# Optimization experiments

Measured on AMD Instinct MI355X. Metric: run time of the kernel, lower is better.

The kernel has to match this reference:

```python
import jax, jax.numpy as jnp
from jax import lax
import numpy as np

EPS = 1e-10
LAMBDA = 0.7  # adaptive_attention_selector: H=64>16 -> 0.0, then C=320>64 -> max(0.0, 0.7)


def delu(x, p=10.0):
    # p*relu(x) + (exp(p*min(x,0)) - 1) + 1  ==  p*relu(x) + exp(p*(x - relu(x)))
    x1 = jax.nn.relu(x)
    return p * x1 + jnp.exp(p * (x - x1))


def conv1x1(x, w, b):
    # x: (B,C,H,W), w: (O,C), b: (O,)
    return jnp.einsum('oc,bchw->bohw', w, x) + b[None, :, None, None]


def conv3x3(x, w, b):
    y = lax.conv_general_dilated(x, w, (1, 1), ((1, 1), (1, 1)),
                                 dimension_numbers=('NCHW', 'OIHW', 'NCHW'))
    return y + b[None, :, None, None]


def _forward(swin_feat, resnet_feat, w_swin, b_swin, w_res, b_res,
             aq_w, aq_b, ak_w, ak_b, av_w, av_b, ad1_w, ad1_b, ad3_w, ad3_b, a_gamma,
             lq_w, lq_b, lk_w, lk_b, lv_w, lv_b, ld1_w, ld1_b, ld3_w, ld3_b, l_gamma,
             wc_w, wc_b):
    sa = conv1x1(swin_feat, w_swin, b_swin)
    ra = conv1x1(resnet_feat, w_res, b_res)
    x = jnp.concatenate([sa, ra], axis=1)           # (B, C=320, H, W)
    B, C, H, W = x.shape
    N = H * W

    # ---- SelfAttentionV1 (softmax bmm output is dead code in the source; only the kv path survives) ----
    q = jnp.swapaxes(conv1x1(x, aq_w, aq_b).reshape(B, -1, N), 1, 2)   # (B, N, C8)
    k = conv1x1(x, ak_w, ak_b).reshape(B, -1, N)                        # (B, C8, N)
    v = conv1x1(x, av_w, av_b).reshape(B, C, N)                         # (B, C, N)
    kv = jnp.einsum('bmn,bcn->bmc', k, v)                               # (B, C8, C)
    norm = 1.0 / jnp.einsum('bnc,bc->bn', q, jnp.sum(k, axis=-1) + EPS) # (B, N)
    wv = jnp.einsum('bnm,bmc,bn->bcn', q, kv, norm).reshape(B, C, H, W)
    d1 = conv1x1(x, ad1_w, ad1_b)
    d3 = conv3x3(x, ad3_w, ad3_b)
    # weight_value = wv + d1 + d3; out = weight_value + d1 + d3 (dconvs added twice in the source)
    attn_out = x + a_gamma * (wv + 2.0 * (d1 + d3))

    # ---- LinearSelfAttention (delu feature map) ----
    ql = delu(conv1x1(x, lq_w, lq_b).reshape(B, C, N))                  # (B, C, N)
    kl = delu(conv1x1(x, lk_w, lk_b).reshape(B, C, N))                  # (B, C, N)
    vl = conv1x1(x, lv_w, lv_b).reshape(B, C, N)                        # (B, C, N)
    energy = jnp.einsum('bmn,bcn->bmc', ql, kl)                         # (B, C, C)
    kv_l = kl * vl                                                      # (B, C, N)
    norm_l = 1.0 / (jnp.einsum('bmc,bcn->bn', energy, kl) + EPS)        # (B, N)
    att_l = jnp.einsum('bmc,bcn,bn->bcn', energy, kv_l, norm_l).reshape(B, C, H, W)
    d1l = conv1x1(x, ld1_w, ld1_b)
    d3l = conv3x3(x, ld3_w, ld3_b)
    lin_out = x + l_gamma * (att_l + d1l + d3l)

    # ---- dynamic blend (lambda is statically 0.7 for these shapes) + residual + compress ----
    out = LAMBDA * attn_out + (1.0 - LAMBDA) * lin_out + x
    return conv1x1(out, wc_w, wc_b)                                     # (B, 160, H, W)


def setup_inputs():
    key = jax.random.key(0)
    ks = iter(jax.random.split(key, 40))

    def randn(shape, scale=1.0):
        return scale * jax.random.normal(next(ks), shape, dtype=jnp.float32)

    B, H, W = 4, 64, 64
    D, C8, S, R = 320, 40, 192, 128
    ws = 0.05  # weight init scale
    return {
        'swin_feat': randn((B, S, H, W)),
        'resnet_feat': randn((B, R, H, W)),
        'w_swin': randn((S, S), ws), 'b_swin': jnp.zeros((S,), jnp.float32),
        'w_res': randn((R, R), ws), 'b_res': jnp.zeros((R,), jnp.float32),
        'aq_w': randn((C8, D), ws), 'aq_b': jnp.zeros((C8,), jnp.float32),
        'ak_w': randn((C8, D), ws), 'ak_b': jnp.zeros((C8,), jnp.float32),
        'av_w': randn((D, D), ws), 'av_b': jnp.zeros((D,), jnp.float32),
        'ad1_w': randn((D, D), ws), 'ad1_b': jnp.zeros((D,), jnp.float32),
        'ad3_w': randn((D, D, 3, 3), ws / 3.0), 'ad3_b': jnp.zeros((D,), jnp.float32),
        'a_gamma': jnp.full((1,), 0.5, jnp.float32),
        'lq_w': randn((D, D), ws), 'lq_b': jnp.zeros((D,), jnp.float32),
        'lk_w': randn((D, D), ws), 'lk_b': jnp.zeros((D,), jnp.float32),
        'lv_w': randn((D, D), ws), 'lv_b': jnp.zeros((D,), jnp.float32),
        'ld1_w': randn((D, D), ws), 'ld1_b': jnp.zeros((D,), jnp.float32),
        'ld3_w': randn((D, D, 3, 3), ws / 3.0), 'ld3_b': jnp.zeros((D,), jnp.float32),
        'l_gamma': jnp.full((1,), 0.5, jnp.float32),
        'wc_w': randn((D // 2, D), ws), 'wc_b': jnp.zeros((D // 2,), jnp.float32),
    }


def reference(swin_feat, resnet_feat, w_swin, b_swin, w_res, b_res,
              aq_w, aq_b, ak_w, ak_b, av_w, av_b, ad1_w, ad1_b, ad3_w, ad3_b, a_gamma,
              lq_w, lq_b, lk_w, lk_b, lv_w, lv_b, ld1_w, ld1_b, ld3_w, ld3_b, l_gamma,
              wc_w, wc_b):
    return _forward(swin_feat, resnet_feat, w_swin, b_swin, w_res, b_res,
                    aq_w, aq_b, ak_w, ak_b, av_w, av_b, ad1_w, ad1_b, ad3_w, ad3_b, a_gamma,
                    lq_w, lq_b, lk_w, lk_b, lv_w, lv_b, ld1_w, ld1_b, ld3_w, ld3_b, l_gamma,
                    wc_w, wc_b)
```

## Files before the change

kernel.cpp:

```cpp
#include <hip/hip_runtime.h>
#include <stdint.h>

#define B4 4
#define NPIX 4096

typedef short sh8 __attribute__((ext_vector_type(8)));
typedef float f4 __attribute__((ext_vector_type(4)));

__device__ __forceinline__ float delu_f(float v){
  return v > 0.f ? __fmaf_rn(10.f, v, 1.f) : __expf(10.f*v);
}
__device__ __forceinline__ unsigned short f2bf(float f){
  unsigned u = __float_as_uint(f);
  u += 0x7fffu + ((u>>16)&1u);
  return (unsigned short)(u>>16);
}
__device__ __forceinline__ float bf2f(unsigned short h){
  return __uint_as_float(((unsigned)h)<<16);
}

__global__ __launch_bounds__(256) void gemm_f32(
    const float* __restrict__ W, const float* __restrict__ bias,
    const float* __restrict__ X, long xStride, int ldX,
    float* __restrict__ Out, long outStride, int ldOut,
    int M, int K)
{
  __shared__ float Wt[16][64];
  __shared__ float Xt[16][64];
  const int b  = blockIdx.z;
  const int m0 = blockIdx.y * 64;
  const int n0 = blockIdx.x * 64;
  const int tid = threadIdx.x;
  const int tc = tid & 15, tr = tid >> 4;
  const int wm = tid >> 2, wk = (tid & 3) << 2;
  const int xk = tid >> 4, xn = (tid & 15) << 2;
  const float* Xb = X + (long)b * xStride;
  float acc[4][4] = {};

  for (int k0 = 0; k0 < K; k0 += 16) {
    float4 wv4;
    if (m0 + wm < M) wv4 = *reinterpret_cast<const float4*>(W + (long)(m0+wm)*K + k0 + wk);
    else wv4 = make_float4(0.f,0.f,0.f,0.f);
    Wt[wk+0][wm] = wv4.x; Wt[wk+1][wm] = wv4.y; Wt[wk+2][wm] = wv4.z; Wt[wk+3][wm] = wv4.w;
    *reinterpret_cast<float4*>(&Xt[xk][xn]) =
        *reinterpret_cast<const float4*>(Xb + (long)(k0+xk)*ldX + n0 + xn);
    __syncthreads();
    #pragma unroll
    for (int kk = 0; kk < 16; ++kk) {
      float4 a4 = *reinterpret_cast<const float4*>(&Wt[kk][tr<<2]);
      float4 b4 = *reinterpret_cast<const float4*>(&Xt[kk][tc<<2]);
      float av[4] = {a4.x,a4.y,a4.z,a4.w};
      float bv[4] = {b4.x,b4.y,b4.z,b4.w};
      #pragma unroll
      for (int i=0;i<4;i++)
        #pragma unroll
        for (int j=0;j<4;j++) acc[i][j] = __fmaf_rn(av[i], bv[j], acc[i][j]);
    }
    __syncthreads();
  }

  #pragma unroll
  for (int i=0;i<4;i++){
    int m = m0 + (tr<<2) + i;
    if (m < M) {
      float bv = bias ? bias[m] : 0.f;
      float r[4];
      #pragma unroll
      for (int j=0;j<4;j++) r[j] = acc[i][j] + bv;
      *reinterpret_cast<float4*>(Out + (long)b*outStride + (long)m*ldOut + n0 + (tc<<2)) =
          make_float4(r[0],r[1],r[2],r[3]);
    }
  }
}

template<int EP, int SPLIT>
__global__ __launch_bounds__(256) void gemm_mfma(
    const unsigned short* __restrict__ Whi, const unsigned short* __restrict__ Wlo,
    const float* __restrict__ bias,
    const unsigned short* __restrict__ Xhi, const unsigned short* __restrict__ Xlo,
    float* __restrict__ Out, long outStride, float* __restrict__ qsum)
{
  __shared__ unsigned short Ah[64][40];
  __shared__ unsigned short Bh[128][40];
  __shared__ unsigned short Al[SPLIT?64:8][40];
  __shared__ unsigned short Bl[SPLIT?128:8][40];
  const int b  = blockIdx.z;
  const int m0 = blockIdx.y * 64;
  const int n0 = blockIdx.x * 128;
  const int tid = threadIdx.x;
  const int sRow = tid >> 2, sK = (tid & 3) << 3;
  const int lane = tid & 63, w = tid >> 6;
  const int wr = w >> 1, wc = w & 1;
  const int fr = lane & 15, fko = (lane >> 4) << 3;

  f4 z4 = {0.f,0.f,0.f,0.f};
  f4 acc[2][4];
  #pragma unroll
  for (int mf=0; mf<2; mf++)
    #pragma unroll
    for (int nf=0; nf<4; nf++) acc[mf][nf] = z4;

  for (int k0 = 0; k0 < 320; k0 += 32) {
    *reinterpret_cast<sh8*>(&Ah[sRow][sK]) =
        *reinterpret_cast<const sh8*>(Whi + (long)(m0+sRow)*320 + k0 + sK);
    if (SPLIT)
      *reinterpret_cast<sh8*>(&Al[sRow][sK]) =
          *reinterpret_cast<const sh8*>(Wlo + (long)(m0+sRow)*320 + k0 + sK);
    #pragma unroll
    for (int r=0; r<2; r++){
      int row = r*64 + sRow;
      long src = ((long)b*NPIX + n0 + row)*320 + k0 + sK;
      *reinterpret_cast<sh8*>(&Bh[row][sK]) = *reinterpret_cast<const sh8*>(Xhi + src);
      if (SPLIT)
        *reinterpret_cast<sh8*>(&Bl[row][sK]) = *reinterpret_cast<const sh8*>(Xlo + src);
    }
    __syncthreads();
    sh8 aH[2], bH[4];
    #pragma unroll
    for (int mf=0; mf<2; mf++)
      aH[mf] = *reinterpret_cast<const sh8*>(&Ah[wr*32 + mf*16 + fr][fko]);
    #pragma unroll
    for (int nf=0; nf<4; nf++)
      bH[nf] = *reinterpret_cast<const sh8*>(&Bh[wc*64 + nf*16 + fr][fko]);
    #pragma unroll
    for (int mf=0; mf<2; mf++)
      #pragma unroll
      for (int nf=0; nf<4; nf++)
        acc[mf][nf] = __builtin_amdgcn_mfma_f32_16x16x32_bf16(aH[mf], bH[nf], acc[mf][nf], 0,0,0);
    if (SPLIT){
      sh8 aL[2], bL[4];
      #pragma unroll
      for (int mf=0; mf<2; mf++)
        aL[mf] = *reinterpret_cast<const sh8*>(&Al[wr*32 + mf*16 + fr][fko]);
      #pragma unroll
      for (int nf=0; nf<4; nf++)
        bL[nf] = *reinterpret_cast<const sh8*>(&Bl[wc*64 + nf*16 + fr][fko]);
      #pragma unroll
      for (int mf=0; mf<2; mf++)
        #pragma unroll
        for (int nf=0; nf<4; nf++){
          acc[mf][nf] = __builtin_amdgcn_mfma_f32_16x16x32_bf16(aL[mf], bH[nf], acc[mf][nf], 0,0,0);
          acc[mf][nf] = __builtin_amdgcn_mfma_f32_16x16x32_bf16(aH[mf], bL[nf], acc[mf][nf], 0,0,0);
        }
    }
    __syncthreads();
  }

  const int orow0 = m0 + wr*32;
  const int ocol  = n0 + wc*64;
  if (EP == 2){
    #pragma unroll
    for (int nf=0; nf<4; nf++){
      float s = 0.f;
      #pragma unroll
      for (int mf=0; mf<2; mf++)
        #pragma unroll
        for (int r=0; r<4; r++)
          s += delu_f(acc[mf][nf][r] + bias[orow0 + mf*16 + ((lane>>4)<<2) + r]);
      s += __shfl_xor(s, 16, 64);
      s += __shfl_xor(s, 32, 64);
      if (lane < 16) atomicAdd(&qsum[(long)b*NPIX + ocol + nf*16 + fr], s);
    }
  } else {
    #pragma unroll
    for (int mf=0; mf<2; mf++)
      #pragma unroll
      for (int r=0; r<4; r++){
        int row = orow0 + mf*16 + ((lane>>4)<<2) + r;
        float bv = bias ? bias[row] : 0.f;
        #pragma unroll
        for (int nf=0; nf<4; nf++){
          float v = acc[mf][nf][r] + bv;
          if (EP == 1) v = delu_f(v);
          Out[(long)b*outStride + (long)row*NPIX + ocol + nf*16 + fr] = v;
        }
      }
  }
}

__global__ __launch_bounds__(256) void xbuild_mfma(
    const unsigned short* __restrict__ inThi, const unsigned short* __restrict__ inTlo,
    int cOff, int K,
    const unsigned short* __restrict__ Wh, const unsigned short* __restrict__ Wl,
    const float* __restrict__ bias, int outC, int tOff,
    unsigned short* __restrict__ xTh, unsigned short* __restrict__ xTl)
{
  __shared__ unsigned short Ah[64][40];
  __shared__ unsigned short Bh[128][40];
  __shared__ unsigned short Al[64][40];
  __shared__ unsigned short Bl[128][40];
  const int b  = blockIdx.z;
  const int m0 = blockIdx.y * 64;
  const int n0 = blockIdx.x * 128;
  const int tid = threadIdx.x;
  const int sRow = tid >> 2, sK = (tid & 3) << 3;
  const int lane = tid & 63, w = tid >> 6;
  const int wr = w >> 1, wc = w & 1;
  const int fr = lane & 15, fko = (lane >> 4) << 3;

  f4 z4 = {0.f,0.f,0.f,0.f};
  f4 acc[2][4];
  #pragma unroll
  for (int mf=0; mf<2; mf++)
    #pragma unroll
    for (int nf=0; nf<4; nf++) acc[mf][nf] = z4;

  for (int k0 = 0; k0 < K; k0 += 32) {
    long asrc = ((long)b*NPIX + m0 + sRow)*320 + cOff + k0 + sK;
    *reinterpret_cast<sh8*>(&Ah[sRow][sK]) = *reinterpret_cast<const sh8*>(inThi + asrc);
    *reinterpret_cast<sh8*>(&Al[sRow][sK]) = *reinterpret_cast<const sh8*>(inTlo + asrc);
    #pragma unroll
    for (int r=0; r<2; r++){
      int row = r*64 + sRow;
      sh8 vh = {0,0,0,0,0,0,0,0}, vl = {0,0,0,0,0,0,0,0};
      if (n0 + row < outC){
        vh = *reinterpret_cast<const sh8*>(Wh + (long)(n0+row)*K + k0 + sK);
        vl = *reinterpret_cast<const sh8*>(Wl + (long)(n0+row)*K + k0 + sK);
      }
      *reinterpret_cast<sh8*>(&Bh[row][sK]) = vh;
      *reinterpret_cast<sh8*>(&Bl[row][sK]) = vl;
    }
    __syncthreads();
    sh8 aH[2], aL[2], bH[4], bL[4];
    #pragma unroll
    for (int mf=0; mf<2; mf++){
      aH[mf] = *reinterpret_cast<const sh8*>(&Ah[wr*32 + mf*16 + fr][fko]);
      aL[mf] = *reinterpret_cast<const sh8*>(&Al[wr*32 + mf*16 + fr][fko]);
    }
    #pragma unroll
    for (int nf=0; nf<4; nf++){
      bH[nf] = *reinterpret_cast<const sh8*>(&Bh[wc*64 + nf*16 + fr][fko]);
      bL[nf] = *reinterpret_cast<const sh8*>(&Bl[wc*64 + nf*16 + fr][fko]);
    }
    #pragma unroll
    for (int mf=0; mf<2; mf++)
      #pragma unroll
      for (int nf=0; nf<4; nf++){
        acc[mf][nf] = __builtin_amdgcn_mfma_f32_16x16x32_bf16(aH[mf], bH[nf], acc[mf][nf], 0,0,0);
        acc[mf][nf] = __builtin_amdgcn_mfma_f32_16x16x32_bf16(aH[mf], bL[nf], acc[mf][nf], 0,0,0);
        acc[mf][nf] = __builtin_amdgcn_mfma_f32_16x16x32_bf16(aL[mf], bH[nf], acc[mf][nf], 0,0,0);
      }
    __syncthreads();
  }

  const int opix0 = m0 + wr*32;
  const int ocol  = n0 + wc*64;
  #pragma unroll
  for (int mf=0; mf<2; mf++)
    #pragma unroll
    for (int r=0; r<4; r++){
      int pix = opix0 + mf*16 + ((lane>>4)<<2) + r;
      #pragma unroll
      for (int nf=0; nf<4; nf++){
        int col = ocol + nf*16 + fr;
        if (col < outC){
          float v = acc[mf][nf][r] + bias[col];
          unsigned short h = f2bf(v);
          long o = ((long)b*NPIX + pix)*320 + tOff + col;
          xTh[o] = h;
          xTl[o] = f2bf(v - bf2f(h));
        }
      }
    }
}

__global__ __launch_bounds__(256) void kvp_mfma(
    const float* __restrict__ proj1, const float* __restrict__ q8f,
    float* __restrict__ kvp)
{
  __shared__ unsigned short Ah[64][40];
  __shared__ unsigned short Bh[128][40];
  __shared__ unsigned short Al[64][40];
  __shared__ unsigned short Bl[128][40];
  const int b = blockIdx.z;
  const int o0 = blockIdx.x * 128;
  const int kbase = blockIdx.y * 128;
  const int tid = threadIdx.x;
  const int sRow = tid >> 2, sK = (tid & 3) << 3;
  const int lane = tid & 63, w = tid >> 6;
  const int wr = w >> 1, wc = w & 1;
  const int fr = lane & 15, fko = (lane >> 4) << 3;
  const float* k8 = q8f + ((long)b*128 + 40)*NPIX;
  const float* vp = proj1 + (long)b*(320L*NPIX);

  f4 z4 = {0.f,0.f,0.f,0.f};
  f4 acc[2][4];
  #pragma unroll
  for (int mf=0; mf<2; mf++)
    #pragma unroll
    for (int nf=0; nf<4; nf++) acc[mf][nf] = z4;

  for (int k0 = 0; k0 < 128; k0 += 32) {
    {
      float vv[8] = {0,0,0,0,0,0,0,0};
      if (sRow < 40){
        float4 a4 = *reinterpret_cast<const float4*>(k8 + (long)sRow*NPIX + kbase + k0 + sK);
        float4 b4 = *reinterpret_cast<const float4*>(k8 + (long)sRow*NPIX + kbase + k0 + sK + 4);
        vv[0]=a4.x; vv[1]=a4.y; vv[2]=a4.z; vv[3]=a4.w;
        vv[4]=b4.x; vv[5]=b4.y; vv[6]=b4.z; vv[7]=b4.w;
      }
      #pragma unroll
      for (int i=0;i<8;i++){
        unsigned short h = f2bf(vv[i]);
        Ah[sRow][sK+i] = h;
        Al[sRow][sK+i] = f2bf(vv[i] - bf2f(h));
      }
    }
    #pragma unroll
    for (int r=0;r<2;r++){
      int row = r*64 + sRow;
      int o = o0 + row;
      float vv[8] = {0,0,0,0,0,0,0,0};
      if (o < 160){
        float4 v4a = *reinterpret_cast<const float4*>(vp + (long)o*NPIX + kbase + k0 + sK);
        float4 v4b = *reinterpret_cast<const float4*>(vp + (long)o*NPIX + kbase + k0 + sK + 4);
        vv[0]=v4a.x; vv[1]=v4a.y; vv[2]=v4a.z; vv[3]=v4a.w;
        vv[4]=v4b.x; vv[5]=v4b.y; vv[6]=v4b.z; vv[7]=v4b.w;
      }
      #pragma unroll
      for (int i=0;i<8;i++){
        unsigned short h = f2bf(vv[i]);
        Bh[row][sK+i] = h;
        Bl[row][sK+i] = f2bf(vv[i] - bf2f(h));
      }
    }
    __syncthreads();
    sh8 aH[2], aL[2], bH[4], bL[4];
    #pragma unroll
    for (int mf=0; mf<2; mf++){
      aH[mf] = *reinterpret_cast<const sh8*>(&Ah[wr*32 + mf*16 + fr][fko]);
      aL[mf] = *reinterpret_cast<const sh8*>(&Al[wr*32 + mf*16 + fr][fko]);
    }
    #pragma unroll
    for (int nf=0; nf<4; nf++){
      bH[nf] = *reinterpret_cast<const sh8*>(&Bh[wc*64 + nf*16 + fr][fko]);
      bL[nf] = *reinterpret_cast<const sh8*>(&Bl[wc*64 + nf*16 + fr][fko]);
    }
    #pragma unroll
    for (int mf=0; mf<2; mf++)
      #pragma unroll
      for (int nf=0; nf<4; nf++){
        acc[mf][nf] = __builtin_amdgcn_mfma_f32_16x16x32_bf16(aH[mf], bH[nf], acc[mf][nf], 0,0,0);
        acc[mf][nf] = __builtin_amdgcn_mfma_f32_16x16x32_bf16(aH[mf], bL[nf], acc[mf][nf], 0,0,0);
        acc[mf][nf] = __builtin_amdgcn_mfma_f32_16x16x32_bf16(aL[mf], bH[nf], acc[mf][nf], 0,0,0);
      }
    __syncthreads();
  }

  const int orow0 = wr*32;
  const int ocol  = o0 + wc*64;
  #pragma unroll
  for (int mf=0; mf<2; mf++)
    #pragma unroll
    for (int r=0; r<4; r++){
      int row = orow0 + mf*16 + ((lane>>4)<<2) + r;
      if (row < 40){
        #pragma unroll
        for (int nf=0; nf<4; nf++){
          int col = ocol + nf*16 + fr;
          if (col < 160)
            atomicAdd(&kvp[((long)b*40 + row)*160 + col], acc[mf][nf][r]);
        }
      }
    }
}

__global__ __launch_bounds__(256) void final_mfma(
    const unsigned short* __restrict__ W2h,
    const unsigned short* __restrict__ pT,
    const float* __restrict__ kvp,
    const float* __restrict__ q8f,
    const float* __restrict__ proj1,
    const float* __restrict__ norm_a, const float* __restrict__ norm_l,
    const float* __restrict__ ag, const float* __restrict__ lg,
    float* __restrict__ Out)
{
  __shared__ unsigned short Ah[64][40];
  __shared__ unsigned short Bh[128][40];
  __shared__ unsigned short Al[64][40];
  __shared__ unsigned short Bl[128][40];
  const int b  = blockIdx.z;
  const int m0 = blockIdx.y * 64;
  const int n0 = blockIdx.x * 128;
  const int tid = threadIdx.x;
  const int sRow = tid >> 2, sK = (tid & 3) << 3;
  const int lane = tid & 63, w = tid >> 6;
  const int wr = w >> 1, wc = w & 1;
  const int fr = lane & 15, fko = (lane >> 4) << 3;

  f4 z4 = {0.f,0.f,0.f,0.f};
  f4 acc1[2][4], acc2[2][4];
  #pragma unroll
  for (int mf=0; mf<2; mf++)
    #pragma unroll
    for (int nf=0; nf<4; nf++){ acc1[mf][nf] = z4; acc2[mf][nf] = z4; }

  for (int k0 = 0; k0 < 320; k0 += 32) {
    sh8 av = {0,0,0,0,0,0,0,0};
    if (m0 + sRow < 160)
      av = *reinterpret_cast<const sh8*>(W2h + ((long)b*160 + m0 + sRow)*320 + k0 + sK);
    *reinterpret_cast<sh8*>(&Ah[sRow][sK]) = av;
    #pragma unroll
    for (int r=0; r<2; r++){
      int row = r*64 + sRow;
      *reinterpret_cast<sh8*>(&Bh[row][sK]) =
          *reinterpret_cast<const sh8*>(pT + ((long)b*NPIX + n0 + row)*320 + k0 + sK);
    }
    __syncthreads();
    sh8 aH[2], bH[4];
    #pragma unroll
    for (int mf=0; mf<2; mf++)
      aH[mf] = *reinterpret_cast<const sh8*>(&Ah[wr*32 + mf*16 + fr][fko]);
    #pragma unroll
    for (int nf=0; nf<4; nf++)
      bH[nf] = *reinterpret_cast<const sh8*>(&Bh[wc*64 + nf*16 + fr][fko]);
    #pragma unroll
    for (int mf=0; mf<2; mf++)
      #pragma unroll
      for (int nf=0; nf<4; nf++)
        acc1[mf][nf] = __builtin_amdgcn_mfma_f32_16x16x32_bf16(aH[mf], bH[nf], acc1[mf][nf], 0,0,0);
    __syncthreads();
  }

  for (int k0 = 0; k0 < 64; k0 += 32) {
    {
      int m = m0 + sRow;
      #pragma unroll
      for (int i=0;i<8;i++){
        int kk = k0 + sK + i;
        float v = (kk < 40 && m < 160) ? kvp[((long)b*40 + kk)*160 + m] : 0.f;
        unsigned short h = f2bf(v);
        Ah[sRow][sK+i] = h;
        Al[sRow][sK+i] = f2bf(v - bf2f(h));
      }
    }
    #pragma unroll
    for (int r=0; r<2; r++){
      int row = r*64 + sRow;
      int pix = n0 + row;
      #pragma unroll
      for (int i=0;i<8;i++){
        int kk = k0 + sK + i;
        float v = (kk < 40) ? q8f[((long)b*128 + kk)*NPIX + pix] : 0.f;
        unsigned short h = f2bf(v);
        Bh[row][sK+i] = h;
        Bl[row][sK+i] = f2bf(v - bf2f(h));
      }
    }
    __syncthreads();
    sh8 aH[2], aL[2], bH[4], bL[4];
    #pragma unroll
    for (int mf=0; mf<2; mf++){
      aH[mf] = *reinterpret_cast<const sh8*>(&Ah[wr*32 + mf*16 + fr][fko]);
      aL[mf] = *reinterpret_cast<const sh8*>(&Al[wr*32 + mf*16 + fr][fko]);
    }
    #pragma unroll
    for (int nf=0; nf<4; nf++){
      bH[nf] = *reinterpret_cast<const sh8*>(&Bh[wc*64 + nf*16 + fr][fko]);
      bL[nf] = *reinterpret_cast<const sh8*>(&Bl[wc*64 + nf*16 + fr][fko]);
    }
    #pragma unroll
    for (int mf=0; mf<2; mf++)
      #pragma unroll
      for (int nf=0; nf<4; nf++){
        acc2[mf][nf] = __builtin_amdgcn_mfma_f32_16x16x32_bf16(aH[mf], bH[nf], acc2[mf][nf], 0,0,0);
        acc2[mf][nf] = __builtin_amdgcn_mfma_f32_16x16x32_bf16(aH[mf], bL[nf], acc2[mf][nf], 0,0,0);
        acc2[mf][nf] = __builtin_amdgcn_mfma_f32_16x16x32_bf16(aL[mf], bH[nf], acc2[mf][nf], 0,0,0);
      }
    __syncthreads();
  }

  const float cA = 0.7f*ag[0], cL = 0.3f*lg[0];
  const int orow0 = m0 + wr*32;
  const int ocol  = n0 + wc*64;
  #pragma unroll
  for (int mf=0; mf<2; mf++)
    #pragma unroll
    for (int r=0; r<4; r++){
      int row = orow0 + mf*16 + ((lane>>4)<<2) + r;
      if (row < 160){
        const float* oa = proj1 + (long)b*(320L*NPIX) + (long)(160+row)*NPIX;
        #pragma unroll
        for (int nf=0; nf<4; nf++){
          int col = ocol + nf*16 + fr;
          Out[((long)b*160 + row)*NPIX + col] =
              oa[col] + cL*norm_l[(long)b*NPIX+col]*acc1[mf][nf][r]
                      + cA*norm_a[(long)b*NPIX+col]*acc2[mf][nf][r];
        }
      }
    }
}

__global__ __launch_bounds__(256) void conv_mfma(
    const unsigned short* __restrict__ Wd3,
    const unsigned short* __restrict__ Xhi,
    float* __restrict__ Out)
{
  __shared__ unsigned short Ah[64][296];
  __shared__ unsigned short Bs[4*66*40];
  const int b  = blockIdx.z;
  const int m0 = blockIdx.y * 64;
  const int n0 = blockIdx.x * 128;
  const int h0 = n0 >> 6;
  const int tid = threadIdx.x;
  const int lane = tid & 63, w = tid >> 6;
  const int wr = w >> 1, wc = w & 1;
  const int fr = lane & 15, fko = (lane >> 4) << 3;

  f4 z4 = {0.f,0.f,0.f,0.f};
  f4 acc[2][4];
  #pragma unroll
  for (int mf=0; mf<2; mf++)
    #pragma unroll
    for (int nf=0; nf<4; nf++) acc[mf][nf] = z4;

  const int sr = tid >> 6;
  const int sw = tid & 63;
  const int hp = h0 - 1 + sr;
  const bool rowok = (hp >= 0) && (hp < 64);
  if (tid < 32){
    int r = tid >> 3;
    int ws = (tid & 4) ? 65 : 0;
    int j = tid & 3;
    sh8 z = {0,0,0,0,0,0,0,0};
    *reinterpret_cast<sh8*>(&Bs[(r*66 + ws)*40 + j*8]) = z;
  }

  const int arow = tid >> 2;
  const int acc8 = (tid & 3) << 3;

  for (int c0 = 0; c0 < 320; c0 += 32){
    #pragma unroll
    for (int t=0; t<9; t++)
      *reinterpret_cast<sh8*>(&Ah[arow][t*32 + acc8]) =
          *reinterpret_cast<const sh8*>(Wd3 + (long)(m0+arow)*2880 + t*320 + c0 + acc8);
    {
      const unsigned short* src = Xhi + ((long)b*NPIX + hp*64 + sw)*320 + c0;
      unsigned short* dst = &Bs[(sr*66 + sw + 1)*40];
      sh8 z = {0,0,0,0,0,0,0,0};
      #pragma unroll
      for (int j=0;j<4;j++){
        sh8 v = z;
        if (rowok) v = *reinterpret_cast<const sh8*>(src + j*8);
        *reinterpret_cast<sh8*>(dst + j*8) = v;
      }
    }
    __syncthreads();
    #pragma unroll
    for (int t=0; t<9; t++){
      const int dh = t/3 - 1, dw = t%3 - 1;
      sh8 aH[2], bH[4];
      #pragma unroll
      for (int mf=0; mf<2; mf++)
        aH[mf] = *reinterpret_cast<const sh8*>(&Ah[wr*32 + mf*16 + fr][t*32 + fko]);
      #pragma unroll
      for (int nf=0; nf<4; nf++){
        int np = wc*64 + nf*16 + fr;
        int lr = (np >> 6) + dh + 1;
        int lw = (np & 63) + dw + 1;
        bH[nf] = *reinterpret_cast<const sh8*>(&Bs[(lr*66 + lw)*40 + fko]);
      }
      #pragma unroll
      for (int mf=0; mf<2; mf++)
        #pragma unroll
        for (int nf=0; nf<4; nf++)
          acc[mf][nf] = __builtin_amdgcn_mfma_f32_16x16x32_bf16(aH[mf], bH[nf], acc[mf][nf], 0,0,0);
    }
    __syncthreads();
  }

  const int orow0 = m0 + wr*32;
  const int ocol  = n0 + wc*64;
  #pragma unroll
  for (int mf=0; mf<2; mf++)
    #pragma unroll
    for (int r=0; r<4; r++){
      int row = orow0 + mf*16 + ((lane>>4)<<2) + r;
      if (row < 160){
        #pragma unroll
        for (int nf=0; nf<4; nf++){
          long o = ((long)b*160 + row)*NPIX + ocol + nf*16 + fr;
          Out[o] += acc[mf][nf][r];
        }
      }
    }
}

__global__ void compose1_kernel(const float* __restrict__ av_w, const float* __restrict__ ad1_w,
    const float* __restrict__ ld1_w, const float* __restrict__ wc_w,
    const float* __restrict__ ag, const float* __restrict__ lg, float* __restrict__ Wbig1)
{
  int idx = blockIdx.x*256 + threadIdx.x;
  if (idx >= 320*320) return;
  int r = idx / 320, c = idx % 320;
  float cD = 1.4f*ag[0], cL = 0.3f*lg[0];
  if (r < 160) {
    float s = 0.f;
    for (int j=0;j<320;j++) s += wc_w[r*320+j]*av_w[j*320+c];
    Wbig1[idx] = s;
  } else {
    int o = r - 160;
    float s1 = 0.f, s2 = 0.f;
    for (int j=0;j<320;j++){
      float w = wc_w[o*320+j];
      s1 += w*ad1_w[j*320+c];
      s2 += w*ld1_w[j*320+c];
    }
    Wbig1[idx] = 2.f*wc_w[o*320+c] + cD*s1 + cL*s2;
  }
}

__global__ void bias1_kernel(const float* __restrict__ av_b, const float* __restrict__ ad1_b,
    const float* __restrict__ ad3_b, const float* __restrict__ ld1_b, const float* __restrict__ ld3_b,
    const float* __restrict__ wc_w, const float* __restrict__ wc_b,
    const float* __restrict__ ag, const float* __restrict__ lg, float* __restrict__ bias1)
{
  int r = blockIdx.x*64 + threadIdx.x;
  if (r >= 320) return;
  float cD = 1.4f*ag[0], cL = 0.3f*lg[0];
  if (r < 160){
    float s = 0.f;
    for (int j=0;j<320;j++) s += wc_w[r*320+j]*av_b[j];
    bias1[r] = s;
  } else {
    int o = r - 160;
    float s = wc_b[o];
    for (int j=0;j<320;j++){
      float w = wc_w[o*320+j];
      s += cD*w*(ad1_b[j]+ad3_b[j]) + cL*w*(ld1_b[j]+ld3_b[j]);
    }
    bias1[r] = s;
  }
}

__global__ void composeqk_kernel(const float* __restrict__ aq_w, const float* __restrict__ aq_b,
    const float* __restrict__ ak_w, const float* __restrict__ ak_b,
    const float* __restrict__ w_swin, const float* __restrict__ b_swin,
    const float* __restrict__ w_res, const float* __restrict__ b_res,
    double* __restrict__ Wsw, double* __restrict__ Wres, double* __restrict__ bqk)
{
  int idx = blockIdx.x*256 + threadIdx.x;
  if (idx < 80*192){
    int m = idx/192, j = idx%192;
    const float* aw = (m < 40) ? aq_w + m*320 : ak_w + (m-40)*320;
    double s = 0.0;
    for (int i=0;i<192;i++) s += (double)aw[i]*(double)w_swin[i*192+j];
    Wsw[idx] = s;
  }
  int idx2 = idx - 80*192;
  if (idx2 >= 0 && idx2 < 80*128){
    int m = idx2/128, j = idx2%128;
    const float* aw = (m < 40) ? aq_w + m*320 + 192 : ak_w + (m-40)*320 + 192;
    double s = 0.0;
    for (int i=0;i<128;i++) s += (double)aw[i]*(double)w_res[i*128+j];
    Wres[idx2] = s;
  }
  int idx3 = idx - 80*192 - 80*128;
  if (idx3 >= 0 && idx3 < 80){
    int m = idx3;
    const float* aw = (m < 40) ? aq_w + m*320 : ak_w + (m-40)*320;
    double s = (double)((m < 40) ? aq_b[m] : ak_b[m-40]);
    for (int i=0;i<192;i++) s += (double)aw[i]*(double)b_swin[i];
    for (int i=0;i<128;i++) s += (double)aw[192+i]*(double)b_res[i];
    bqk[m] = s;
  }
}

__global__ void t1_kernel(const float* __restrict__ ad3_w, const float* __restrict__ ld3_w,
    const float* __restrict__ ag, const float* __restrict__ lg, float* __restrict__ Wmix)
{
  long idx = (long)blockIdx.x*256 + threadIdx.x;
  if (idx >= 2880L*320) return;
  int k = (int)(idx / 320), c = (int)(idx % 320);
  int t = k / 320, j = k % 320;
  float cD = 1.4f*ag[0], cL = 0.3f*lg[0];
  long src = (long)(j*320 + c)*9 + t;
  Wmix[idx] = cD*ad3_w[src] + cL*ld3_w[src];
}

__global__ void cvtqk_kernel(const double* __restrict__ Wsw, const double* __restrict__ Wres,
    const double* __restrict__ bqk,
    unsigned short* __restrict__ Wqkh, unsigned short* __restrict__ Wqkl,
    float* __restrict__ biasqk)
{
  int idx = blockIdx.x*256 + threadIdx.x;
  if (idx < 128*320){
    int row = idx / 320, col = idx % 320;
    double v = 0.0;
    if (row < 80) v = (col < 192) ? Wsw[row*192+col] : Wres[row*128+(col-192)];
    float f = (float)v;
    unsigned short h = f2bf(f);
    Wqkh[idx] = h;
    Wqkl[idx] = f2bf(f - bf2f(h));
  }
  if (idx < 128) biasqk[idx] = (idx < 80) ? (float)bqk[idx] : 0.f;
}

__global__ void cvt_bf16_kernel(const float* __restrict__ src, unsigned short* __restrict__ dst, int n){
  int i = blockIdx.x*256 + threadIdx.x;
  if (i < n) dst[i] = f2bf(src[i]);
}
__global__ void cvt_split_kernel(const float* __restrict__ src,
    unsigned short* __restrict__ hi, unsigned short* __restrict__ lo, int n){
  int i = blockIdx.x*256 + threadIdx.x;
  if (i < n){
    float v = src[i];
    unsigned short h = f2bf(v);
    hi[i] = h;
    lo[i] = f2bf(v - bf2f(h));
  }
}
__global__ void cvt_pad_kernel(const float* __restrict__ src, unsigned short* __restrict__ dst){
  int i = blockIdx.x*256 + threadIdx.x;
  if (i >= 192*2880) return;
  int row = i / 2880;
  dst[i] = (row < 160) ? f2bf(src[i]) : (unsigned short)0;
}

__global__ __launch_bounds__(256) void inT_kernel(
    const float* __restrict__ swin, const float* __restrict__ resnet,
    const double* __restrict__ wdad, double* __restrict__ dabuf,
    unsigned short* __restrict__ inThi, unsigned short* __restrict__ inTlo)
{
  __shared__ float t[64][65];
  __shared__ double redD[4][64];
  const int b = blockIdx.z, ct = blockIdx.y, n0 = blockIdx.x*64;
  const float* src; int C, cs0;
  if (ct < 3){ src = swin;   C = 192; cs0 = ct*64; }
  else       { src = resnet; C = 128; cs0 = (ct-3)*64; }
  const int dst0 = ct*64;
  const int tid = threadIdx.x;
  #pragma unroll
  for (int it=0; it<16; ++it){
    int idx = it*256 + tid;
    int c = idx >> 6, n = idx & 63;
    t[c][n] = src[((long)b*C + cs0 + c)*NPIX + n0 + n];
  }
  __syncthreads();
  {
    int cg = tid >> 6, n = tid & 63;
    double s = 0.0;
    #pragma unroll
    for (int j=0;j<16;j++){
      int c = cg*16 + j;
      s += wdad[b*320 + dst0 + c] * (double)t[c][n];
    }
    redD[cg][n] = s;
  }
  __syncthreads();
  if (tid < 64){
    double s = redD[0][tid]+redD[1][tid]+redD[2][tid]+redD[3][tid];
    atomicAdd(&dabuf[(long)b*NPIX + n0 + tid], s);
  }
  #pragma unroll
  for (int it=0; it<16; ++it){
    int idx = it*256 + tid;
    int n = idx >> 6, c = idx & 63;
    float v = t[c][n];
    unsigned short h = f2bf(v);
    long o = ((long)b*NPIX + n0 + n)*320 + dst0 + c;
    inThi[o] = h;
    inTlo[o] = f2bf(v - bf2f(h));
  }
}

__global__ __launch_bounds__(256) void pT_kernel(
    const float* __restrict__ projL, const float* __restrict__ colsum,
    unsigned short* __restrict__ pT, float* __restrict__ dlbuf)
{
  __shared__ float t[64][65];
  __shared__ float css[64];
  __shared__ float redF[4][64];
  const int b = blockIdx.z, c0 = blockIdx.y*64, n0 = blockIdx.x*64;
  const float* kl = projL + (long)b*(640L*NPIX);
  const float* vl = kl + 320L*NPIX;
  const int tid = threadIdx.x;
  if (tid < 64) css[tid] = colsum[b*320 + c0 + tid];
  __syncthreads();
  float sdl = 0.f;
  #pragma unroll
  for (int it=0; it<16; ++it){
    int idx = it*256 + tid;
    int c = idx >> 6, n = idx & 63;
    long s = (long)(c0+c)*NPIX + n0 + n;
    float klv = kl[s];
    t[c][n] = klv*vl[s];
    sdl = __fmaf_rn(css[c], klv, sdl);
  }
  redF[tid>>6][tid&63] = sdl;
  __syncthreads();
  if (tid < 64)
    atomicAdd(&dlbuf[(long)b*NPIX + n0 + tid],
              redF[0][tid]+redF[1][tid]+redF[2][tid]+redF[3][tid]);
  #pragma unroll
  for (int it=0; it<16; ++it){
    int idx = it*256 + tid;
    int n = idx >> 6, c = idx & 63;
    pT[((long)b*NPIX + n0 + n)*320 + c0 + c] = f2bf(t[c][n]);
  }
}

__global__ void normfin_kernel(const double* __restrict__ dabuf, const double* __restrict__ cdad,
    const float* __restrict__ dlbuf, float* __restrict__ norm_a, float* __restrict__ norm_l)
{
  int i = blockIdx.x*256 + threadIdx.x;
  if (i >= B4*NPIX) return;
  int b = i >> 12;
  norm_a[i] = (float)(1.0/(dabuf[i] + cdad[b]));
  norm_l[i] = 1.f/(dlbuf[i] + 1e-10f);
}

__global__ void w2_kernel(const float* __restrict__ wc_w, const float* __restrict__ colsum,
    unsigned short* __restrict__ W2h)
{
  int idx = blockIdx.x*256 + threadIdx.x;
  if (idx >= B4*160*320) return;
  int b = idx / (160*320);
  int rem = idx - b*160*320;
  int c = rem % 320;
  W2h[idx] = f2bf(wc_w[rem]*colsum[b*320+c]);
}

__global__ __launch_bounds__(256) void chsum_kernel(
    const float* __restrict__ swin, const float* __restrict__ resnet,
    double* __restrict__ chsumd)
{
  int b = blockIdx.y, c = blockIdx.x;
  const float* row = (c < 192) ? swin + ((long)b*192 + c)*NPIX
                               : resnet + ((long)b*128 + (c-192))*NPIX;
  double s = 0.0;
  for (int n = threadIdx.x; n < NPIX; n += 256) s += (double)row[n];
  __shared__ double sd[256];
  sd[threadIdx.x] = s; __syncthreads();
  for (int o=128; o; o>>=1){ if (threadIdx.x < o) sd[threadIdx.x] += sd[threadIdx.x+o]; __syncthreads(); }
  if (threadIdx.x == 0) chsumd[b*320+c] = sd[0];
}

__global__ __launch_bounds__(320) void skda_kernel(
    const double* __restrict__ Wsw, const double* __restrict__ Wres,
    const double* __restrict__ bqk, const double* __restrict__ chsumd,
    double* __restrict__ wdad, double* __restrict__ cdad)
{
  int b = blockIdx.x;
  __shared__ double sk[40];
  int tid = threadIdx.x;
  if (tid < 40){
    int m = 40 + tid;
    double s = 4096.0 * bqk[m];
    for (int j=0;j<192;j++) s += Wsw[m*192+j]*chsumd[b*320+j];
    for (int j=0;j<128;j++) s += Wres[m*128+j]*chsumd[b*320+192+j];
    sk[tid] = s + 1e-10;
  }
  __syncthreads();
  {
    int c = tid;
    double s = 0.0;
    if (c < 192){ for (int m=0;m<40;m++) s += sk[m]*Wsw[m*192+c]; }
    else        { for (int m=0;m<40;m++) s += sk[m]*Wres[m*128+(c-192)]; }
    wdad[b*320+c] = s;
  }
  if (tid == 0){
    double s = 0.0;
    for (int m=0;m<40;m++) s += sk[m]*bqk[m];
    cdad[b] = s;
  }
}

__global__ void colsum_kernel(const float* __restrict__ projL, const float* __restrict__ qsum,
    float* __restrict__ colsum)
{
  int b = blockIdx.y, c = blockIdx.x;
  const float* kl = projL + (long)b*640*NPIX + (long)c*NPIX;
  const float* qs = qsum + (long)b*NPIX;
  double s = 0.0;
  for (int n=threadIdx.x; n<NPIX; n+=256) s += (double)kl[n]*(double)qs[n];
  __shared__ double sd[256];
  sd[threadIdx.x] = s; __syncthreads();
  for (int o=128; o; o>>=1){ if (threadIdx.x < o) sd[threadIdx.x] += sd[threadIdx.x+o]; __syncthreads(); }
  if (threadIdx.x == 0) colsum[b*320+c] = (float)sd[0];
}

extern "C" void kernel_launch(void* const* d_in, const int* in_sizes, int n_in,
                              void* d_out, int out_size, void* d_ws, size_t ws_size,
                              hipStream_t stream)
{
  const float* swin   = (const float*)d_in[0];
  const float* resnet = (const float*)d_in[1];
  const float* w_swin = (const float*)d_in[2];
  const float* b_swin = (const float*)d_in[3];
  const float* w_res  = (const float*)d_in[4];
  const float* b_res  = (const float*)d_in[5];
  const float* aq_w = (const float*)d_in[6];
  const float* aq_b = (const float*)d_in[7];
  const float* ak_w = (const float*)d_in[8];
  const float* ak_b = (const float*)d_in[9];
  const float* av_w = (const float*)d_in[10];
  const float* av_b = (const float*)d_in[11];
  const float* ad1_w = (const float*)d_in[12];
  const float* ad1_b = (const float*)d_in[13];
  const float* ad3_w = (const float*)d_in[14];
  const float* ad3_b = (const float*)d_in[15];
  const float* ag    = (const float*)d_in[16];
  const float* lq_w = (const float*)d_in[17];
  const float* lq_b = (const float*)d_in[18];
  const float* lk_w = (const float*)d_in[19];
  const float* lk_b = (const float*)d_in[20];
  const float* lv_w = (const float*)d_in[21];
  const float* lv_b = (const float*)d_in[22];
  const float* ld1_w = (const float*)d_in[23];
  const float* ld1_b = (const float*)d_in[24];
  const float* ld3_w = (const float*)d_in[25];
  const float* ld3_b = (const float*)d_in[26];
  const float* lg    = (const float*)d_in[27];
  const float* wc_w = (const float*)d_in[28];
  const float* wc_b = (const float*)d_in[29];
  float* out = (float*)d_out;

  char* p = (char*)d_ws;
  double* Wsw   = (double*)p; p += (size_t)80*192*8;
  double* Wres  = (double*)p; p += (size_t)80*128*8;
  double* bqk   = (double*)p; p += (size_t)80*8;
  double* chsumd= (double*)p; p += (size_t)B4*320*8;
  double* wdad  = (double*)p; p += (size_t)B4*320*8;
  double* cdad  = (double*)p; p += (size_t)B4*8;
  double* dabuf = (double*)p; p += (size_t)B4*NPIX*8;
  float* dlbuf  = (float*)p;  p += (size_t)B4*NPIX*4;
  float* q8f    = (float*)p;  p += (size_t)B4*128*NPIX*4;
  float* proj1  = (float*)p;  p += (size_t)B4*320*NPIX*4;
  float* projL  = (float*)p;  p += (size_t)B4*640*NPIX*4;
  float* qsum   = (float*)p;  p += (size_t)B4*NPIX*4;
  float* norm_a = (float*)p;  p += (size_t)B4*NPIX*4;
  float* norm_l = (float*)p;  p += (size_t)B4*NPIX*4;
  float* colsum = (float*)p;  p += (size_t)B4*320*4;
  float* kvp    = (float*)p;  p += (size_t)B4*40*160*4;
  float* Wbig1  = (float*)p;  p += (size_t)320*320*4;
  float* bias1  = (float*)p;  p += (size_t)320*4;
  float* Wmix   = (float*)p;  p += (size_t)2880*320*4;
  float* Wd3eff = (float*)p;  p += (size_t)160*2880*4;
  float* biasqk = (float*)p;  p += (size_t)128*4;
  p = (char*)(((uintptr_t)p + 255) & ~(uintptr_t)255);
  unsigned short* xTh  = (unsigned short*)p; p += (size_t)B4*NPIX*320*2;
  unsigned short* xTl  = (unsigned short*)p; p += (size_t)B4*NPIX*320*2;
  unsigned short* Wb1h = (unsigned short*)p; p += (size_t)320*320*2;
  unsigned short* Wb1l = (unsigned short*)p; p += (size_t)320*320*2;
  unsigned short* lqh  = (unsigned short*)p; p += (size_t)320*320*2;
  unsigned short* lkh  = (unsigned short*)p; p += (size_t)320*320*2;
  unsigned short* lvh  = (unsigned short*)p; p += (size_t)320*320*2;
  unsigned short* Wd3b = (unsigned short*)p; p += (size_t)192*2880*2;
  unsigned short* wswh = (unsigned short*)p; p += (size_t)192*192*2;
  unsigned short* wswl = (unsigned short*)p; p += (size_t)192*192*2;
  unsigned short* wrsh = (unsigned short*)p; p += (size_t)128*128*2;
  unsigned short* wrsl = (unsigned short*)p; p += (size_t)128*128*2;
  unsigned short* Wqkh = (unsigned short*)p; p += (size_t)128*320*2;
  unsigned short* Wqkl = (unsigned short*)p; p += (size_t)128*320*2;
  if ((size_t)(p - (char*)d_ws) > ws_size) return;

  unsigned short* inThi = (unsigned short*)projL;
  unsigned short* inTlo = inThi + (size_t)B4*NPIX*320;
  unsigned short* pT = xTl;
  unsigned short* W2h = (unsigned short*)Wmix;

  hipMemsetAsync(qsum, 0, (size_t)B4*NPIX*4, stream);
  hipMemsetAsync(kvp,  0, (size_t)B4*40*160*4, stream);
  hipMemsetAsync(dabuf, 0, (size_t)B4*NPIX*8, stream);
  hipMemsetAsync(dlbuf, 0, (size_t)B4*NPIX*4, stream);

  composeqk_kernel<<<(80*192 + 80*128 + 80 + 255)/256, 256, 0, stream>>>(
      aq_w, aq_b, ak_w, ak_b, w_swin, b_swin, w_res, b_res, Wsw, Wres, bqk);
  compose1_kernel<<<(320*320 + 255)/256, 256, 0, stream>>>(av_w, ad1_w, ld1_w, wc_w, ag, lg, Wbig1);
  bias1_kernel<<<5, 64, 0, stream>>>(av_b, ad1_b, ad3_b, ld1_b, ld3_b, wc_w, wc_b, ag, lg, bias1);
  t1_kernel<<<(2880*320 + 255)/256, 256, 0, stream>>>(ad3_w, ld3_w, ag, lg, Wmix);
  gemm_f32<<<dim3(5,3,9), 256, 0, stream>>>(wc_w, nullptr, Wmix, 320L*320, 320,
      Wd3eff, 320, 2880, 160, 320);

  cvt_split_kernel<<<(320*320 + 255)/256, 256, 0, stream>>>(Wbig1, Wb1h, Wb1l, 320*320);
  cvt_bf16_kernel<<<(320*320 + 255)/256, 256, 0, stream>>>(lq_w, lqh, 320*320);
  cvt_bf16_kernel<<<(320*320 + 255)/256, 256, 0, stream>>>(lk_w, lkh, 320*320);
  cvt_bf16_kernel<<<(320*320 + 255)/256, 256, 0, stream>>>(lv_w, lvh, 320*320);
  cvt_pad_kernel<<<(192*2880 + 255)/256, 256, 0, stream>>>(Wd3eff, Wd3b);
  cvt_split_kernel<<<(192*192 + 255)/256, 256, 0, stream>>>(w_swin, wswh, wswl, 192*192);
  cvt_split_kernel<<<(128*128 + 255)/256, 256, 0, stream>>>(w_res, wrsh, wrsl, 128*128);
  cvtqk_kernel<<<(128*320 + 255)/256, 256, 0, stream>>>(Wsw, Wres, bqk, Wqkh, Wqkl, biasqk);

  chsum_kernel<<<dim3(320,4), 256, 0, stream>>>(swin, resnet, chsumd);
  skda_kernel<<<4, 320, 0, stream>>>(Wsw, Wres, bqk, chsumd, wdad, cdad);

  inT_kernel<<<dim3(64,5,4), 256, 0, stream>>>(swin, resnet, wdad, dabuf, inThi, inTlo);
  xbuild_mfma<<<dim3(2,64,4), 256, 0, stream>>>(inThi, inTlo, 0, 192,
      wswh, wswl, b_swin, 192, 0, xTh, xTl);
  xbuild_mfma<<<dim3(1,64,4), 256, 0, stream>>>(inThi, inTlo, 192, 128,
      wrsh, wrsl, b_res, 128, 192, xTh, xTl);
  gemm_mfma<0,1><<<dim3(32,2,4), 256, 0, stream>>>(Wqkh, Wqkl, biasqk, inThi, inTlo,
      q8f, 128L*NPIX, nullptr);

  gemm_mfma<2,0><<<dim3(32,5,4), 256, 0, stream>>>(lqh, nullptr, lq_b, xTh, nullptr,
      nullptr, 0, qsum);
  gemm_mfma<1,0><<<dim3(32,5,4), 256, 0, stream>>>(lkh, nullptr, lk_b, xTh, nullptr,
      projL, 640L*NPIX, nullptr);
  gemm_mfma<0,0><<<dim3(32,5,4), 256, 0, stream>>>(lvh, nullptr, lv_b, xTh, nullptr,
      projL + 320L*NPIX, 640L*NPIX, nullptr);
  gemm_mfma<0,1><<<dim3(32,5,4), 256, 0, stream>>>(Wb1h, Wb1l, bias1, xTh, xTl,
      proj1, 320L*NPIX, nullptr);

  kvp_mfma<<<dim3(2,32,4), 256, 0, stream>>>(proj1, q8f, kvp);
  colsum_kernel<<<dim3(320,4), 256, 0, stream>>>(projL, qsum, colsum);

  pT_kernel<<<dim3(64,5,4), 256, 0, stream>>>(projL, colsum, pT, dlbuf);
  normfin_kernel<<<(B4*NPIX + 255)/256, 256, 0, stream>>>(dabuf, cdad, dlbuf, norm_a, norm_l);
  w2_kernel<<<(B4*160*320 + 255)/256, 256, 0, stream>>>(wc_w, colsum, W2h);

  final_mfma<<<dim3(32,3,4), 256, 0, stream>>>(W2h, pT, kvp, q8f, proj1,
                                               norm_a, norm_l, ag, lg, out);
  conv_mfma<<<dim3(32,3,4), 256, 0, stream>>>(Wd3b, xTh, out);
}
```

Measured before the change: 354.8 us.

## Merge linear-attention q/k/v GEMMs into one launch and prefetch conv tiles

Replaces the three separate q/k/v projection GEMM launches with a single launch over 960 output rows. It relies on the lq/lk/lv bf16 weights being contiguous and on a concatenated bias buffer, and picks the epilogue (delu row-sum, delu store, plain store) per 320-row segment. The 3x3 conv kernel now prefetches the next channel slice of weights and input into registers while the current slice is computed. It also regroups the LDS input tile by 8-channel group, which changes its bank access pattern. The aim is to cut launch count and tail effects and to hide global load latency, at the cost of more registers in the conv kernel.

```diff
diff --git a/kernel.cpp b/kernel.cpp
--- a/kernel.cpp
+++ b/kernel.cpp
@@ -148,18 +148,37 @@
 
   const int orow0 = m0 + wr*32;
   const int ocol  = n0 + wc*64;
-  if (EP == 2){
-    #pragma unroll
-    for (int nf=0; nf<4; nf++){
-      float s = 0.f;
+  if (EP == 3){
+    const int seg = m0 / 320;
+    if (seg == 0){
+      #pragma unroll
+      for (int nf=0; nf<4; nf++){
+        float s = 0.f;
+        #pragma unroll
+        for (int mf=0; mf<2; mf++)
+          #pragma unroll
+          for (int r=0; r<4; r++)
+            s += delu_f(acc[mf][nf][r] + bias[orow0 + mf*16 + ((lane>>4)<<2) + r]);
+        s += __shfl_xor(s, 16, 64);
+        s += __shfl_xor(s, 32, 64);
+        if (lane < 16) atomicAdd(&qsum[(long)b*NPIX + ocol + nf*16 + fr], s);
+      }
+    } else {
+      const int mseg0 = m0 - seg*320 + wr*32;
+      long base = (long)b*outStride + (seg == 2 ? 320L*NPIX : 0);
       #pragma unroll
       for (int mf=0; mf<2; mf++)
         #pragma unroll
-        for (int r=0; r<4; r++)
-          s += delu_f(acc[mf][nf][r] + bias[orow0 + mf*16 + ((lane>>4)<<2) + r]);
-      s += __shfl_xor(s, 16, 64);
-      s += __shfl_xor(s, 32, 64);
-      if (lane < 16) atomicAdd(&qsum[(long)b*NPIX + ocol + nf*16 + fr], s);
+        for (int r=0; r<4; r++){
+          int rowI = mseg0 + mf*16 + ((lane>>4)<<2) + r;
+          float bv = bias[seg*320 + rowI];
+          #pragma unroll
+          for (int nf=0; nf<4; nf++){
+            float v = acc[mf][nf][r] + bv;
+            if (seg == 1) v = delu_f(v);
+            Out[base + (long)rowI*NPIX + ocol + nf*16 + fr] = v;
+          }
+        }
     }
   } else {
     #pragma unroll
@@ -171,7 +190,6 @@
         #pragma unroll
         for (int nf=0; nf<4; nf++){
           float v = acc[mf][nf][r] + bv;
-          if (EP == 1) v = delu_f(v);
           Out[(long)b*outStride + (long)row*NPIX + ocol + nf*16 + fr] = v;
         }
       }
@@ -496,8 +514,8 @@
     const unsigned short* __restrict__ Xhi,
     float* __restrict__ Out)
 {
-  __shared__ unsigned short Ah[64][296];
-  __shared__ unsigned short Bs[4*66*40];
+  __shared__ unsigned short Ah[64][292];
+  __shared__ unsigned short Bs[4*265*8];
   const int b  = blockIdx.z;
   const int m0 = blockIdx.y * 64;
   const int n0 = blockIdx.x * 128;
@@ -505,7 +523,8 @@
   const int tid = threadIdx.x;
   const int lane = tid & 63, w = tid >> 6;
   const int wr = w >> 1, wc = w & 1;
-  const int fr = lane & 15, fko = (lane >> 4) << 3;
+  const int fr = lane & 15, fg = lane >> 4;
+  const int fko = fg << 3;
 
   f4 z4 = {0.f,0.f,0.f,0.f};
   f4 acc[2][4];
@@ -518,31 +537,48 @@
   const int sw = tid & 63;
   const int hp = h0 - 1 + sr;
   const bool rowok = (hp >= 0) && (hp < 64);
+  const sh8 zero8 = {0,0,0,0,0,0,0,0};
   if (tid < 32){
     int r = tid >> 3;
     int ws = (tid & 4) ? 65 : 0;
-    int j = tid & 3;
-    sh8 z = {0,0,0,0,0,0,0,0};
-    *reinterpret_cast<sh8*>(&Bs[(r*66 + ws)*40 + j*8]) = z;
+    int g = tid & 3;
+    *reinterpret_cast<sh8*>(&Bs[((size_t)g*265 + r*66 + ws)*8]) = zero8;
   }
 
   const int arow = tid >> 2;
-  const int acc8 = (tid & 3) << 3;
+  const int acol = (tid & 3) << 3;
+
+  sh8 aReg[9], bReg[4];
+  {
+    const unsigned short* wsrc = Wd3 + (long)(m0+arow)*2880 + acol;
+    #pragma unroll
+    for (int t=0;t<9;t++) aReg[t] = *reinterpret_cast<const sh8*>(wsrc + t*320);
+    const unsigned short* bsrc = Xhi + ((long)b*NPIX + hp*64 + sw)*320;
+    #pragma unroll
+    for (int g=0; g<4; g++){
+      sh8 v = zero8;
+      if (rowok) v = *reinterpret_cast<const sh8*>(bsrc + g*8);
+      bReg[g] = v;
+    }
+  }
 
   for (int c0 = 0; c0 < 320; c0 += 32){
     #pragma unroll
-    for (int t=0; t<9; t++)
-      *reinterpret_cast<sh8*>(&Ah[arow][t*32 + acc8]) =
-          *reinterpret_cast<const sh8*>(Wd3 + (long)(m0+arow)*2880 + t*320 + c0 + acc8);
-    {
-      const unsigned short* src = Xhi + ((long)b*NPIX + hp*64 + sw)*320 + c0;
-      unsigned short* dst = &Bs[(sr*66 + sw + 1)*40];
-      sh8 z = {0,0,0,0,0,0,0,0};
-      #pragma unroll
-      for (int j=0;j<4;j++){
-        sh8 v = z;
-        if (rowok) v = *reinterpret_cast<const sh8*>(src + j*8);
-        *reinterpret_cast<sh8*>(dst + j*8) = v;
+    for (int t=0;t<9;t++)
+      *reinterpret_cast<sh8*>(&Ah[arow][t*32 + acol]) = aReg[t];
+    #pragma unroll
+    for (int g=0; g<4; g++)
+      *reinterpret_cast<sh8*>(&Bs[((size_t)g*265 + sr*66 + sw + 1)*8]) = bReg[g];
+    if (c0 + 32 < 320){
+      const unsigned short* wsrc = Wd3 + (long)(m0+arow)*2880 + c0 + 32 + acol;
+      #pragma unroll
+      for (int t=0;t<9;t++) aReg[t] = *reinterpret_cast<const sh8*>(wsrc + t*320);
+      const unsigned short* bsrc = Xhi + ((long)b*NPIX + hp*64 + sw)*320 + c0 + 32;
+      #pragma unroll
+      for (int g=0; g<4; g++){
+        sh8 v = zero8;
+        if (rowok) v = *reinterpret_cast<const sh8*>(bsrc + g*8);
+        bReg[g] = v;
       }
     }
     __syncthreads();
@@ -558,7 +594,7 @@
         int np = wc*64 + nf*16 + fr;
         int lr = (np >> 6) + dh + 1;
         int lw = (np & 63) + dw + 1;
-        bH[nf] = *reinterpret_cast<const sh8*>(&Bs[(lr*66 + lw)*40 + fko]);
+        bH[nf] = *reinterpret_cast<const sh8*>(&Bs[((size_t)fg*265 + lr*66 + lw)*8]);
       }
       #pragma unroll
       for (int mf=0; mf<2; mf++)
@@ -715,6 +751,13 @@
   if (i >= 192*2880) return;
   int row = i / 2880;
   dst[i] = (row < 160) ? f2bf(src[i]) : (unsigned short)0;
+}
+__global__ void bias3_kernel(const float* __restrict__ a, const float* __restrict__ b_,
+    const float* __restrict__ c, float* __restrict__ o){
+  int i = blockIdx.x*256 + threadIdx.x;
+  if (i < 320) o[i] = a[i];
+  else if (i < 640) o[i] = b_[i-320];
+  else if (i < 960) o[i] = c[i-640];
 }
 
 __global__ __launch_bounds__(256) void inT_kernel(
@@ -938,6 +981,7 @@
   float* Wmix   = (float*)p;  p += (size_t)2880*320*4;
   float* Wd3eff = (float*)p;  p += (size_t)160*2880*4;
   float* biasqk = (float*)p;  p += (size_t)128*4;
+  float* bias3  = (float*)p;  p += (size_t)960*4;
   p = (char*)(((uintptr_t)p + 255) & ~(uintptr_t)255);
   unsigned short* xTh  = (unsigned short*)p; p += (size_t)B4*NPIX*320*2;
   unsigned short* xTl  = (unsigned short*)p; p += (size_t)B4*NPIX*320*2;
@@ -981,6 +1025,7 @@
   cvt_split_kernel<<<(192*192 + 255)/256, 256, 0, stream>>>(w_swin, wswh, wswl, 192*192);
   cvt_split_kernel<<<(128*128 + 255)/256, 256, 0, stream>>>(w_res, wrsh, wrsl, 128*128);
   cvtqk_kernel<<<(128*320 + 255)/256, 256, 0, stream>>>(Wsw, Wres, bqk, Wqkh, Wqkl, biasqk);
+  bias3_kernel<<<4, 256, 0, stream>>>(lq_b, lk_b, lv_b, bias3);
 
   chsum_kernel<<<dim3(320,4), 256, 0, stream>>>(swin, resnet, chsumd);
   skda_kernel<<<4, 320, 0, stream>>>(Wsw, Wres, bqk, chsumd, wdad, cdad);
@@ -993,12 +1038,8 @@
   gemm_mfma<0,1><<<dim3(32,2,4), 256, 0, stream>>>(Wqkh, Wqkl, biasqk, inThi, inTlo,
       q8f, 128L*NPIX, nullptr);
 
-  gemm_mfma<2,0><<<dim3(32,5,4), 256, 0, stream>>>(lqh, nullptr, lq_b, xTh, nullptr,
-      nullptr, 0, qsum);
-  gemm_mfma<1,0><<<dim3(32,5,4), 256, 0, stream>>>(lkh, nullptr, lk_b, xTh, nullptr,
-      projL, 640L*NPIX, nullptr);
-  gemm_mfma<0,0><<<dim3(32,5,4), 256, 0, stream>>>(lvh, nullptr, lv_b, xTh, nullptr,
-      projL + 320L*NPIX, 640L*NPIX, nullptr);
+  gemm_mfma<3,0><<<dim3(32,15,4), 256, 0, stream>>>(lqh, nullptr, bias3, xTh, nullptr,
+      projL, 640L*NPIX, qsum);
   gemm_mfma<0,1><<<dim3(32,5,4), 256, 0, stream>>>(Wb1h, Wb1l, bias1, xTh, xTl,
       proj1, 320L*NPIX, nullptr);
 
```

Result: faster. 340.3 us (-4.1%).
